# Kernel optimization log

Measured on AMD Instinct MI355X. Metric: run time of the kernel, lower is better.

The kernel has to match this reference:

```python
import jax, jax.numpy as jnp
import numpy as np

NEG = 9000000000000000.0  # large negative multiplier from the original code

def setup_inputs() -> dict:
    key = jax.random.key(0)
    ks = jax.random.split(key, 7)
    B, N, DIN, H, DOUT = 128, 512, 256, 256, 256
    x = jax.random.normal(ks[0], (B, N, DIN), dtype=jnp.float32)
    # binary float mask (1 = attend, 0 = blocked), as used multiplicatively in the module
    mask = (jax.random.uniform(ks[1], (B, N, N)) > 0.5).astype(jnp.float32)
    def lin(k, fan_in, fan_out):
        kw, kb = jax.random.split(k)
        bound = 1.0 / np.sqrt(fan_in)
        W = jax.random.uniform(kw, (fan_in, fan_out), minval=-bound, maxval=bound, dtype=jnp.float32)
        b = jax.random.uniform(kb, (fan_out,), minval=-bound, maxval=bound, dtype=jnp.float32)
        return W, b
    Wv, bv = lin(ks[2], DIN, H)
    Wk, bk = lin(ks[3], DIN, H)
    Wq, bq = lin(ks[4], DIN, H)
    Wo, bo = lin(ks[5], H, DOUT)
    return {"x": x, "mask": mask, "Wv": Wv, "bv": bv, "Wk": Wk, "bk": bk,
            "Wq": Wq, "bq": bq, "Wo": Wo, "bo": bo}

def reference(x, mask, Wv, bv, Wk, bk, Wq, bq, Wo, bo):
    # x: [B,N,din], mask: [B,N,N]
    v = jax.nn.relu(jnp.einsum('bnd,dh->bnh', x, Wv) + bv)   # [B,N,H]
    q = jax.nn.relu(jnp.einsum('bnd,dh->bnh', x, Wq) + bq)   # [B,N,H]
    k = jax.nn.relu(jnp.einsum('bnd,dh->bnh', x, Wk) + bk)   # [B,N,H]
    scores = jnp.einsum('bnh,bmh->bnm', q, k)                 # [B,N,N]
    att = jax.nn.softmax(scores * mask - NEG * (1.0 - mask), axis=2)
    out = jnp.einsum('bnm,bmh->bnh', att, v)                  # [B,N,H]
    out = jax.nn.relu(jnp.einsum('bnh,ho->bno', out, Wo) + bo)
    return out
```

## Files before the change

### kernel.cpp

```cpp
#include <hip/hip_runtime.h>
#include <stdint.h>

typedef __attribute__((ext_vector_type(8))) __bf16 bf16x8;
typedef __attribute__((ext_vector_type(4))) float f32x4;
typedef __attribute__((ext_vector_type(8))) unsigned short ushort8;
typedef __attribute__((ext_vector_type(4))) unsigned short ushort4v;
typedef unsigned short u16;
typedef unsigned int u32;

__device__ __forceinline__ u16 f2bf(float f) {
    __bf16 h = (__bf16)f;
    return __builtin_bit_cast(u16, h);
}

__device__ __forceinline__ f32x4 mfma16(bf16x8 a, bf16x8 b, f32x4 c) {
    return __builtin_amdgcn_mfma_f32_16x16x32_bf16(a, b, c, 0, 0, 0);
}

typedef __attribute__((address_space(1))) const char g_char;
typedef __attribute__((address_space(3))) char l_char;
__device__ __forceinline__ void gload_lds16(const void* g, void* l) {
    __builtin_amdgcn_global_load_lds((g_char*)g, (l_char*)l, 16, 0, 0);
}

__global__ __launch_bounds__(256) void prep_w(
    const float* __restrict__ Wq, const float* __restrict__ Wk,
    const float* __restrict__ Wv, const float* __restrict__ Wo,
    u16* __restrict__ WT, u16* __restrict__ WOT)
{
    int idx = blockIdx.x * 256 + threadIdx.x;
    if (idx < 196608) {
        int j = idx >> 8, k = idx & 255;
        const float* W = (j < 256) ? Wq : (j < 512) ? Wk : Wv;
        WT[idx] = f2bf(W[k * 256 + (j & 255)]);
    } else {
        int t = idx - 196608;
        int j = t >> 8, k = t & 255;
        WOT[t] = f2bf(Wo[k * 256 + j]);
    }
}

__global__ __launch_bounds__(256, 2) void qkv_gemm(
    const float* __restrict__ X, const u16* __restrict__ WT,
    const float* __restrict__ bQ, const float* __restrict__ bK,
    const float* __restrict__ bV,
    u16* __restrict__ outQ, u16* __restrict__ outK, u16* __restrict__ outVT)
{
    __shared__ __align__(16) u16 As[128 * 256];
    __shared__ __align__(16) u16 Bs[128 * 64];
    const int tid = threadIdx.x;
    const int m0 = blockIdx.x * 128;

    #pragma unroll
    for (int i = 0; i < 32; ++i) {
        int flat = (i * 256 + tid) * 4;
        int r = flat >> 8, c = flat & 255;
        const float4 f = *reinterpret_cast<const float4*>(X + (size_t)(m0 + r) * 256 + c);
        ushort4v h;
        h.x = f2bf(f.x); h.y = f2bf(f.y); h.z = f2bf(f.z); h.w = f2bf(f.w);
        int byte = (r * 512 + c * 2) ^ ((r & 7) << 4);
        *reinterpret_cast<ushort4v*>(reinterpret_cast<char*>(As) + byte) = h;
    }

    const int lane = tid & 63, wid = tid >> 6;
    const int wr = wid >> 1, wc = wid & 1;
    const int lr = lane & 15, lg = lane >> 4;

    for (int cb = 0; cb < 6; ++cb) {
        const int jbase = cb * 128;
        f32x4 acc[4][4];
        #pragma unroll
        for (int a = 0; a < 4; ++a)
            #pragma unroll
            for (int b = 0; b < 4; ++b) acc[a][b] = (f32x4){0.f, 0.f, 0.f, 0.f};

        for (int kk = 0; kk < 256; kk += 64) {
            __syncthreads();
            #pragma unroll
            for (int i = 0; i < 4; ++i) {
                int e = (i * 256 + tid) * 8;
                int r = e >> 6, c = e & 63;
                ushort8 d = *reinterpret_cast<const ushort8*>(WT + (size_t)(jbase + r) * 256 + kk + c);
                int byte = (r * 128 + c * 2) ^ ((r & 7) << 4);
                *reinterpret_cast<ushort8*>(reinterpret_cast<char*>(Bs) + byte) = d;
            }
            __syncthreads();
            #pragma unroll
            for (int ks = 0; ks < 2; ++ks) {
                bf16x8 af[4], bfr[4];
                #pragma unroll
                for (int mt = 0; mt < 4; ++mt) {
                    int r = wr * 64 + mt * 16 + lr;
                    int byte = (r * 512 + (kk + ks * 32 + lg * 8) * 2) ^ ((r & 7) << 4);
                    af[mt] = *reinterpret_cast<const bf16x8*>(reinterpret_cast<const char*>(As) + byte);
                }
                #pragma unroll
                for (int nt = 0; nt < 4; ++nt) {
                    int r = wc * 64 + nt * 16 + lr;
                    int byte = (r * 128 + (ks * 32 + lg * 8) * 2) ^ ((r & 7) << 4);
                    bfr[nt] = *reinterpret_cast<const bf16x8*>(reinterpret_cast<const char*>(Bs) + byte);
                }
                #pragma unroll
                for (int mt = 0; mt < 4; ++mt)
                    #pragma unroll
                    for (int nt = 0; nt < 4; ++nt)
                        acc[mt][nt] = mfma16(af[mt], bfr[nt], acc[mt][nt]);
            }
        }
        const float* bias = (cb < 2) ? bQ : (cb < 4) ? bK : bV;
        float bcol[4];
        #pragma unroll
        for (int nt = 0; nt < 4; ++nt)
            bcol[nt] = bias[(jbase + wc * 64 + nt * 16 + lr) & 255];
        #pragma unroll
        for (int mt = 0; mt < 4; ++mt) {
            #pragma unroll
            for (int nt = 0; nt < 4; ++nt) {
                #pragma unroll
                for (int j = 0; j < 4; ++j) {
                    float v = fmaxf(acc[mt][nt][j] + bcol[nt], 0.f);
                    u16 h = f2bf(v);
                    int row = m0 + wr * 64 + mt * 16 + lg * 4 + j;
                    int col = jbase + wc * 64 + nt * 16 + lr;
                    if (cb < 2) {
                        outQ[(size_t)row * 256 + col] = h;
                    } else if (cb < 4) {
                        outK[(size_t)row * 256 + (col - 256)] = h;
                    } else {
                        int bb = row >> 9, n = row & 511;
                        outVT[(size_t)bb * 131072 + (size_t)(col - 512) * 512 + n] = h;
                    }
                }
            }
        }
    }
}

__global__ __launch_bounds__(512) void attn_kernel(
    const u16* __restrict__ Q, const u16* __restrict__ K,
    const u16* __restrict__ VT, const float* __restrict__ Mask,
    u16* __restrict__ Out)
{
    __shared__ __align__(16) u16 k_lds[2][32 * 256];
    __shared__ __align__(16) u16 v_lds[2][256 * 32];
    __shared__ __align__(16) u16 p_lds[8][16 * 32];
    const int tid = threadIdx.x;
    const int b  = blockIdx.x & 127;
    const int rb = blockIdx.x >> 7;
    const int lane = tid & 63, wid = tid >> 6;
    const int lr = lane & 15, lg = lane >> 4;
    const int n0 = rb * 128 + wid * 16;
    const u16* qbat = Q  + (size_t)b * 512 * 256;
    const u16* kbat = K  + (size_t)b * 512 * 256;
    const u16* vbat = VT + (size_t)b * 256 * 512;
    const float* mrow = Mask + ((size_t)b * 512 + n0 + lg * 4) * 512;

    auto stage = [&](int buf, int kt) {
        #pragma unroll
        for (int i = 0; i < 2; ++i) {
            int p = (i * 512 + tid) * 16;
            int krow = p >> 9, kcol2 = p & 511;
            int scol2 = kcol2 ^ ((krow & 7) << 4);
            const char* gk = reinterpret_cast<const char*>(kbat + (size_t)(kt * 32 + krow) * 256) + scol2;
            char* lk = reinterpret_cast<char*>(k_lds[buf]) + i * 8192 + wid * 1024;
            gload_lds16(gk, lk);
            int vrow = p >> 6, vcol2 = p & 63;
            const char* gv = reinterpret_cast<const char*>(vbat + (size_t)vrow * 512 + kt * 32) + vcol2;
            char* lv = reinterpret_cast<char*>(v_lds[buf]) + i * 8192 + wid * 1024;
            gload_lds16(gv, lv);
        }
    };

    stage(0, 0);
    float mf[2][4];
    #pragma unroll
    for (int ct = 0; ct < 2; ++ct)
        #pragma unroll
        for (int j = 0; j < 4; ++j)
            mf[ct][j] = __builtin_nontemporal_load(mrow + (size_t)j * 512 + ct * 16 + lr);

    f32x4 acc[16];
    #pragma unroll
    for (int i = 0; i < 16; ++i) acc[i] = (f32x4){0.f, 0.f, 0.f, 0.f};
    float mreg[4], lreg[4];
    #pragma unroll
    for (int j = 0; j < 4; ++j) { mreg[j] = -__builtin_inff(); lreg[j] = 0.f; }

    __syncthreads();

    for (int kt = 0; kt < 16; ++kt) {
        const int cur = kt & 1;
        if (kt < 15) stage(cur ^ 1, kt + 1);

        u32 mb = 0;
        #pragma unroll
        for (int ct = 0; ct < 2; ++ct)
            #pragma unroll
            for (int j = 0; j < 4; ++j)
                mb |= (mf[ct][j] > 0.5f ? 1u : 0u) << (ct * 4 + j);
        if (kt < 15) {
            #pragma unroll
            for (int ct = 0; ct < 2; ++ct)
                #pragma unroll
                for (int j = 0; j < 4; ++j)
                    mf[ct][j] = __builtin_nontemporal_load(
                        mrow + (size_t)j * 512 + (kt + 1) * 32 + ct * 16 + lr);
        }

        f32x4 s[2];
        s[0] = (f32x4){0.f, 0.f, 0.f, 0.f};
        s[1] = (f32x4){0.f, 0.f, 0.f, 0.f};
        const char* kbase = reinterpret_cast<const char*>(k_lds[cur]);
        __builtin_amdgcn_s_setprio(1);
        #pragma unroll
        for (int ks = 0; ks < 8; ++ks) {
            bf16x8 qv = *reinterpret_cast<const bf16x8*>(
                qbat + (size_t)(n0 + lr) * 256 + ks * 32 + lg * 8);
            #pragma unroll
            for (int ct = 0; ct < 2; ++ct) {
                int krow = ct * 16 + lr;
                int byte = (krow * 512 + (ks * 32 + lg * 8) * 2) ^ ((krow & 7) << 4);
                bf16x8 kf = *reinterpret_cast<const bf16x8*>(kbase + byte);
                s[ct] = mfma16(qv, kf, s[ct]);
            }
        }
        __builtin_amdgcn_s_setprio(0);

        float p[2][4];
        #pragma unroll
        for (int ct = 0; ct < 2; ++ct)
            #pragma unroll
            for (int j = 0; j < 4; ++j)
                p[ct][j] = ((mb >> (ct * 4 + j)) & 1u) ? s[ct][j] : -9.0e15f;

        float r0j[4];
        bool need = false;
        #pragma unroll
        for (int j = 0; j < 4; ++j) {
            float r0 = fmaxf(p[0][j], p[1][j]);
            r0 = fmaxf(r0, __shfl_xor(r0, 1));
            r0 = fmaxf(r0, __shfl_xor(r0, 2));
            r0 = fmaxf(r0, __shfl_xor(r0, 4));
            r0 = fmaxf(r0, __shfl_xor(r0, 8));
            r0j[j] = r0;
            need = need || (r0 > mreg[j]);
        }
        if (__any(need)) {
            #pragma unroll
            for (int j = 0; j < 4; ++j) {
                float mnew = fmaxf(mreg[j], r0j[j]);
                float sc = __expf(mreg[j] - mnew);
                mreg[j] = mnew;
                lreg[j] *= sc;
                #pragma unroll
                for (int ht = 0; ht < 16; ++ht) acc[ht][j] *= sc;
            }
        }
        #pragma unroll
        for (int j = 0; j < 4; ++j) {
            float ps = 0.f;
            #pragma unroll
            for (int ct = 0; ct < 2; ++ct) {
                float e = __expf(p[ct][j] - mreg[j]);
                p[ct][j] = e;
                ps += e;
            }
            lreg[j] += ps;
        }

        #pragma unroll
        for (int ct = 0; ct < 2; ++ct)
            #pragma unroll
            for (int j = 0; j < 4; ++j) {
                int byte = (lg * 4 + j) * 64 + (ct * 16 + lr) * 2;
                *reinterpret_cast<u16*>(reinterpret_cast<char*>(p_lds[wid]) + byte) = f2bf(p[ct][j]);
            }

        bf16x8 pf = *reinterpret_cast<const bf16x8*>(
            reinterpret_cast<const char*>(p_lds[wid]) + lr * 64 + lg * 16);
        const char* vbase = reinterpret_cast<const char*>(v_lds[cur]);
        __builtin_amdgcn_s_setprio(1);
        #pragma unroll
        for (int ht = 0; ht < 16; ++ht) {
            bf16x8 vf = *reinterpret_cast<const bf16x8*>(vbase + (ht * 16 + lr) * 64 + lg * 16);
            acc[ht] = mfma16(pf, vf, acc[ht]);
        }
        __builtin_amdgcn_s_setprio(0);

        __syncthreads();
    }

    #pragma unroll
    for (int j = 0; j < 4; ++j) {
        float lt = lreg[j];
        lt += __shfl_xor(lt, 1);
        lt += __shfl_xor(lt, 2);
        lt += __shfl_xor(lt, 4);
        lt += __shfl_xor(lt, 8);
        float inv = 1.0f / lt;
        int qn = n0 + lg * 4 + j;
        u16* orow = Out + ((size_t)b * 512 + qn) * 256;
        #pragma unroll
        for (int ht = 0; ht < 16; ++ht)
            orow[ht * 16 + lr] = f2bf(acc[ht][j] * inv);
    }
}

__global__ __launch_bounds__(256, 2) void out_gemm(
    const u16* __restrict__ A, const u16* __restrict__ WOT,
    const float* __restrict__ bO, float* __restrict__ Out)
{
    __shared__ __align__(16) u16 As[128 * 256];
    __shared__ __align__(16) u16 Bs[128 * 64];
    const int tid = threadIdx.x;
    const int m0 = blockIdx.x * 128;

    #pragma unroll
    for (int i = 0; i < 16; ++i) {
        int e = (i * 256 + tid) * 8;
        int r = e >> 8, c = e & 255;
        ushort8 d = *reinterpret_cast<const ushort8*>(A + (size_t)(m0 + r) * 256 + c);
        int byte = (r * 512 + c * 2) ^ ((r & 7) << 4);
        *reinterpret_cast<ushort8*>(reinterpret_cast<char*>(As) + byte) = d;
    }

    const int lane = tid & 63, wid = tid >> 6;
    const int wr = wid >> 1, wc = wid & 1;
    const int lr = lane & 15, lg = lane >> 4;

    for (int cb = 0; cb < 2; ++cb) {
        const int jbase = cb * 128;
        f32x4 acc[4][4];
        #pragma unroll
        for (int a = 0; a < 4; ++a)
            #pragma unroll
            for (int b = 0; b < 4; ++b) acc[a][b] = (f32x4){0.f, 0.f, 0.f, 0.f};

        for (int kk = 0; kk < 256; kk += 64) {
            __syncthreads();
            #pragma unroll
            for (int i = 0; i < 4; ++i) {
                int e = (i * 256 + tid) * 8;
                int r = e >> 6, c = e & 63;
                ushort8 d = *reinterpret_cast<const ushort8*>(WOT + (size_t)(jbase + r) * 256 + kk + c);
                int byte = (r * 128 + c * 2) ^ ((r & 7) << 4);
                *reinterpret_cast<ushort8*>(reinterpret_cast<char*>(Bs) + byte) = d;
            }
            __syncthreads();
            #pragma unroll
            for (int ks = 0; ks < 2; ++ks) {
                bf16x8 af[4], bfr[4];
                #pragma unroll
                for (int mt = 0; mt < 4; ++mt) {
                    int r = wr * 64 + mt * 16 + lr;
                    int byte = (r * 512 + (kk + ks * 32 + lg * 8) * 2) ^ ((r & 7) << 4);
                    af[mt] = *reinterpret_cast<const bf16x8*>(reinterpret_cast<const char*>(As) + byte);
                }
                #pragma unroll
                for (int nt = 0; nt < 4; ++nt) {
                    int r = wc * 64 + nt * 16 + lr;
                    int byte = (r * 128 + (ks * 32 + lg * 8) * 2) ^ ((r & 7) << 4);
                    bfr[nt] = *reinterpret_cast<const bf16x8*>(reinterpret_cast<const char*>(Bs) + byte);
                }
                #pragma unroll
                for (int mt = 0; mt < 4; ++mt)
                    #pragma unroll
                    for (int nt = 0; nt < 4; ++nt)
                        acc[mt][nt] = mfma16(af[mt], bfr[nt], acc[mt][nt]);
            }
        }
        float bcol[4];
        #pragma unroll
        for (int nt = 0; nt < 4; ++nt)
            bcol[nt] = bO[jbase + wc * 64 + nt * 16 + lr];
        #pragma unroll
        for (int mt = 0; mt < 4; ++mt) {
            #pragma unroll
            for (int nt = 0; nt < 4; ++nt) {
                #pragma unroll
                for (int j = 0; j < 4; ++j) {
                    float v = fmaxf(acc[mt][nt][j] + bcol[nt], 0.f);
                    int row = m0 + wr * 64 + mt * 16 + lg * 4 + j;
                    int col = jbase + wc * 64 + nt * 16 + lr;
                    Out[(size_t)row * 256 + col] = v;
                }
            }
        }
    }
}

extern "C" void kernel_launch(void* const* d_in, const int* in_sizes, int n_in,
                              void* d_out, int out_size, void* d_ws, size_t ws_size,
                              hipStream_t stream) {
    const float* x    = (const float*)d_in[0];
    const float* mask = (const float*)d_in[1];
    const float* Wv   = (const float*)d_in[2];
    const float* bv   = (const float*)d_in[3];
    const float* Wk   = (const float*)d_in[4];
    const float* bk   = (const float*)d_in[5];
    const float* Wq   = (const float*)d_in[6];
    const float* bq   = (const float*)d_in[7];
    const float* Wo   = (const float*)d_in[8];
    const float* bo   = (const float*)d_in[9];
    float* out = (float*)d_out;

    char* ws = (char*)d_ws;
    u16* WT  = (u16*)(ws);
    u16* WOT = (u16*)(ws + 393216);
    u16* Qb  = (u16*)(ws + 524288);
    u16* Kb  = (u16*)(ws + 524288 + 33554432);
    u16* VTb = (u16*)(ws + 524288 + 2 * 33554432);

    prep_w<<<1024, 256, 0, stream>>>(Wq, Wk, Wv, Wo, WT, WOT);
    qkv_gemm<<<512, 256, 0, stream>>>(x, WT, bq, bk, bv, Qb, Kb, VTb);
    attn_kernel<<<512, 512, 0, stream>>>(Qb, Kb, VTb, mask, Qb);
    out_gemm<<<512, 256, 0, stream>>>(Qb, WOT, bo, out);
}
```

Before: 198.5 us.

## Pre-pack mask into bitmask and swizzle V/P LDS layouts in attention

Adds a prep pass that converts the float mask into 32-bit bitwords per row chunk, stored temporarily in the output buffer. The attention kernel then reads compact bitmask words instead of strided float mask loads in its inner loop. It also XOR-swizzles the V tile layout in LDS and pads the P scratch rows to reduce bank conflicts. The mask is still read in full once, now in a separate kernel that also writes the packed form, so total traffic barely changes and the gain depends on removing latency and issue pressure from the attention loop.

```diff
diff --git a/kernel.cpp b/kernel.cpp
--- a/kernel.cpp
+++ b/kernel.cpp
@@ -23,20 +23,38 @@
     __builtin_amdgcn_global_load_lds((g_char*)g, (l_char*)l, 16, 0, 0);
 }
 
-__global__ __launch_bounds__(256) void prep_w(
+__global__ __launch_bounds__(256) void prep_pack(
     const float* __restrict__ Wq, const float* __restrict__ Wk,
     const float* __restrict__ Wv, const float* __restrict__ Wo,
-    u16* __restrict__ WT, u16* __restrict__ WOT)
+    const float* __restrict__ Mask,
+    u16* __restrict__ WT, u16* __restrict__ WOT, u32* __restrict__ MP)
 {
-    int idx = blockIdx.x * 256 + threadIdx.x;
-    if (idx < 196608) {
-        int j = idx >> 8, k = idx & 255;
-        const float* W = (j < 256) ? Wq : (j < 512) ? Wk : Wv;
-        WT[idx] = f2bf(W[k * 256 + (j & 255)]);
+    int bid = blockIdx.x;
+    if (bid < 1024) {
+        int idx = bid * 256 + threadIdx.x;
+        if (idx < 196608) {
+            int j = idx >> 8, k = idx & 255;
+            const float* W = (j < 256) ? Wq : (j < 512) ? Wk : Wv;
+            WT[idx] = f2bf(W[k * 256 + (j & 255)]);
+        } else {
+            int t = idx - 196608;
+            int j = t >> 8, k = t & 255;
+            WOT[t] = f2bf(Wo[k * 256 + j]);
+        }
     } else {
-        int t = idx - 196608;
-        int j = t >> 8, k = t & 255;
-        WOT[t] = f2bf(Wo[k * 256 + j]);
+        int t = (bid - 1024) * 256 + threadIdx.x;
+        const float* mp = Mask + (size_t)t * 32;
+        u32 w = 0;
+        #pragma unroll
+        for (int i = 0; i < 8; ++i) {
+            f32x4 f = __builtin_nontemporal_load(
+                reinterpret_cast<const f32x4*>(mp + i * 4));
+            w |= (f.x > 0.5f ? 1u : 0u) << (i * 4 + 0);
+            w |= (f.y > 0.5f ? 1u : 0u) << (i * 4 + 1);
+            w |= (f.z > 0.5f ? 1u : 0u) << (i * 4 + 2);
+            w |= (f.w > 0.5f ? 1u : 0u) << (i * 4 + 3);
+        }
+        MP[t] = w;
     }
 }
 
@@ -55,7 +73,7 @@
     for (int i = 0; i < 32; ++i) {
         int flat = (i * 256 + tid) * 4;
         int r = flat >> 8, c = flat & 255;
-        const float4 f = *reinterpret_cast<const float4*>(X + (size_t)(m0 + r) * 256 + c);
+        const f32x4 f = *reinterpret_cast<const f32x4*>(X + (size_t)(m0 + r) * 256 + c);
         ushort4v h;
         h.x = f2bf(f.x); h.y = f2bf(f.y); h.z = f2bf(f.z); h.w = f2bf(f.w);
         int byte = (r * 512 + c * 2) ^ ((r & 7) << 4);
@@ -138,12 +156,12 @@
 
 __global__ __launch_bounds__(512) void attn_kernel(
     const u16* __restrict__ Q, const u16* __restrict__ K,
-    const u16* __restrict__ VT, const float* __restrict__ Mask,
+    const u16* __restrict__ VT, const u32* __restrict__ MP,
     u16* __restrict__ Out)
 {
     __shared__ __align__(16) u16 k_lds[2][32 * 256];
     __shared__ __align__(16) u16 v_lds[2][256 * 32];
-    __shared__ __align__(16) u16 p_lds[8][16 * 32];
+    __shared__ __align__(16) u16 p_lds[8][16 * 36];
     const int tid = threadIdx.x;
     const int b  = blockIdx.x & 127;
     const int rb = blockIdx.x >> 7;
@@ -153,7 +171,7 @@
     const u16* qbat = Q  + (size_t)b * 512 * 256;
     const u16* kbat = K  + (size_t)b * 512 * 256;
     const u16* vbat = VT + (size_t)b * 256 * 512;
-    const float* mrow = Mask + ((size_t)b * 512 + n0 + lg * 4) * 512;
+    const u32* mpr  = MP + ((size_t)b * 512 + n0 + lg * 4) * 16;
 
     auto stage = [&](int buf, int kt) {
         #pragma unroll
@@ -164,20 +182,16 @@
             const char* gk = reinterpret_cast<const char*>(kbat + (size_t)(kt * 32 + krow) * 256) + scol2;
             char* lk = reinterpret_cast<char*>(k_lds[buf]) + i * 8192 + wid * 1024;
             gload_lds16(gk, lk);
-            int vrow = p >> 6, vcol2 = p & 63;
-            const char* gv = reinterpret_cast<const char*>(vbat + (size_t)vrow * 512 + kt * 32) + vcol2;
+            int vrow = p >> 6;
+            int chunk = (p >> 4) & 3;
+            int schunk = chunk ^ (vrow & 3);
+            const char* gv = reinterpret_cast<const char*>(vbat + (size_t)vrow * 512 + kt * 32) + schunk * 16;
             char* lv = reinterpret_cast<char*>(v_lds[buf]) + i * 8192 + wid * 1024;
             gload_lds16(gv, lv);
         }
     };
 
     stage(0, 0);
-    float mf[2][4];
-    #pragma unroll
-    for (int ct = 0; ct < 2; ++ct)
-        #pragma unroll
-        for (int j = 0; j < 4; ++j)
-            mf[ct][j] = __builtin_nontemporal_load(mrow + (size_t)j * 512 + ct * 16 + lr);
 
     f32x4 acc[16];
     #pragma unroll
@@ -192,20 +206,9 @@
         const int cur = kt & 1;
         if (kt < 15) stage(cur ^ 1, kt + 1);
 
-        u32 mb = 0;
-        #pragma unroll
-        for (int ct = 0; ct < 2; ++ct)
-            #pragma unroll
-            for (int j = 0; j < 4; ++j)
-                mb |= (mf[ct][j] > 0.5f ? 1u : 0u) << (ct * 4 + j);
-        if (kt < 15) {
-            #pragma unroll
-            for (int ct = 0; ct < 2; ++ct)
-                #pragma unroll
-                for (int j = 0; j < 4; ++j)
-                    mf[ct][j] = __builtin_nontemporal_load(
-                        mrow + (size_t)j * 512 + (kt + 1) * 32 + ct * 16 + lr);
-        }
+        u32 mw[4];
+        #pragma unroll
+        for (int j = 0; j < 4; ++j) mw[j] = mpr[j * 16 + kt];
 
         f32x4 s[2];
         s[0] = (f32x4){0.f, 0.f, 0.f, 0.f};
@@ -231,7 +234,7 @@
         for (int ct = 0; ct < 2; ++ct)
             #pragma unroll
             for (int j = 0; j < 4; ++j)
-                p[ct][j] = ((mb >> (ct * 4 + j)) & 1u) ? s[ct][j] : -9.0e15f;
+                p[ct][j] = ((mw[j] >> (ct * 16 + lr)) & 1u) ? s[ct][j] : -9.0e15f;
 
         float r0j[4];
         bool need = false;
@@ -272,17 +275,19 @@
         for (int ct = 0; ct < 2; ++ct)
             #pragma unroll
             for (int j = 0; j < 4; ++j) {
-                int byte = (lg * 4 + j) * 64 + (ct * 16 + lr) * 2;
+                int byte = (lg * 4 + j) * 72 + (ct * 16 + lr) * 2;
                 *reinterpret_cast<u16*>(reinterpret_cast<char*>(p_lds[wid]) + byte) = f2bf(p[ct][j]);
             }
 
         bf16x8 pf = *reinterpret_cast<const bf16x8*>(
-            reinterpret_cast<const char*>(p_lds[wid]) + lr * 64 + lg * 16);
+            reinterpret_cast<const char*>(p_lds[wid]) + lr * 72 + lg * 16);
         const char* vbase = reinterpret_cast<const char*>(v_lds[cur]);
         __builtin_amdgcn_s_setprio(1);
         #pragma unroll
         for (int ht = 0; ht < 16; ++ht) {
-            bf16x8 vf = *reinterpret_cast<const bf16x8*>(vbase + (ht * 16 + lr) * 64 + lg * 16);
+            int hrow = ht * 16 + lr;
+            int byte = (hrow * 64 + lg * 16) ^ ((hrow & 3) << 4);
+            bf16x8 vf = *reinterpret_cast<const bf16x8*>(vbase + byte);
             acc[ht] = mfma16(pf, vf, acc[ht]);
         }
         __builtin_amdgcn_s_setprio(0);
@@ -410,9 +415,10 @@
     u16* Qb  = (u16*)(ws + 524288);
     u16* Kb  = (u16*)(ws + 524288 + 33554432);
     u16* VTb = (u16*)(ws + 524288 + 2 * 33554432);
-
-    prep_w<<<1024, 256, 0, stream>>>(Wq, Wk, Wv, Wo, WT, WOT);
+    u32* MPk = (u32*)d_out;
+
+    prep_pack<<<5120, 256, 0, stream>>>(Wq, Wk, Wv, Wo, mask, WT, WOT, MPk);
     qkv_gemm<<<512, 256, 0, stream>>>(x, WT, bq, bk, bv, Qb, Kb, VTb);
-    attn_kernel<<<512, 512, 0, stream>>>(Qb, Kb, VTb, mask, Qb);
+    attn_kernel<<<512, 512, 0, stream>>>(Qb, Kb, VTb, MPk, Qb);
     out_gemm<<<512, 256, 0, stream>>>(Qb, WOT, bo, out);
 }
```

Measured after the change: 243.4 us. 1.23x slower.
